# Kernel optimization log

Measured on AMD Instinct MI355X. Metric: run time of the kernel, lower is better.

## Reference

```python
import jax, jax.numpy as jnp
import numpy as np

B, T, D, H, O = 32768, 96, 7, 3, 7

def setup_inputs() -> dict:
    key = jax.random.key(0)
    ks = jax.random.split(key, 7)
    s_ih = 1.0 / np.sqrt(H)
    inp = {
        "x": jax.random.normal(ks[0], (B, T, D), dtype=jnp.float32),
        # PyTorch nn.LSTM params (gate order i,f,g,o), uniform(-1/sqrt(H), 1/sqrt(H))
        "W_ih": jax.random.uniform(ks[1], (4 * H, D), jnp.float32, -s_ih, s_ih),
        "W_hh": jax.random.uniform(ks[2], (4 * H, H), jnp.float32, -s_ih, s_ih),
        "b_ih": jax.random.uniform(ks[3], (4 * H,), jnp.float32, -s_ih, s_ih),
        "b_hh": jax.random.uniform(ks[4], (4 * H,), jnp.float32, -s_ih, s_ih),
        # nn.Linear(H*T, O*T): weight [out,in]
        "W_lin": jax.random.uniform(ks[5], (O * T, H * T), jnp.float32, -1.0 / np.sqrt(H * T), 1.0 / np.sqrt(H * T)),
        "b_lin": jax.random.uniform(ks[6], (O * T,), jnp.float32, -1.0 / np.sqrt(H * T), 1.0 / np.sqrt(H * T)),
    }
    return inp

def _lstm(x, W_ih, W_hh, b_ih, b_hh):
    b = x.shape[0]
    h0 = jnp.zeros((b, H), x.dtype)
    c0 = jnp.zeros((b, H), x.dtype)
    bias = b_ih + b_hh

    def step(carry, x_t):
        h, c = carry
        gates = x_t @ W_ih.T + h @ W_hh.T + bias  # [b, 4H]
        i, f, g, o = jnp.split(gates, 4, axis=-1)
        i = jax.nn.sigmoid(i)
        f = jax.nn.sigmoid(f)
        g = jnp.tanh(g)
        o = jax.nn.sigmoid(o)
        c = f * c + i * g
        h = o * jnp.tanh(c)
        return (h, c), h

    (_, _), hs = jax.lax.scan(step, (h0, c0), jnp.swapaxes(x, 0, 1))  # hs: [T, b, H]
    return jnp.swapaxes(hs, 0, 1)  # [b, T, H]

def reference(x, W_ih, W_hh, b_ih, b_hh, W_lin, b_lin):
    out = _lstm(x, W_ih, W_hh, b_ih, b_hh)            # [B, T, H]
    out = out.reshape(x.shape[0], -1)                  # [B, T*H]
    out = out @ W_lin.T + b_lin                        # [B, O*T]
    return out.reshape(x.shape)                        # [B, T, D]
```

## Files before the change

### kernel.cpp

```cpp
#include <hip/hip_runtime.h>
#include <stdint.h>

typedef unsigned short u16;
typedef unsigned int u32;
typedef __attribute__((ext_vector_type(8))) __bf16 bf16x8;
typedef __attribute__((ext_vector_type(4))) float f32x4;

#define B_TOT   32768
#define T_SEQ   96
#define D_IN    7
#define K_LIN   288
#define N_LIN   672
#define N_PAD   768

#define LOG2E      1.4426950408889634f
#define TWO_LOG2E  2.8853900817779268f

__device__ __forceinline__ u16 f2bf(float f) {
  u32 u = __builtin_bit_cast(u32, f);
  u += 0x7fffu + ((u >> 16) & 1u);
  return (u16)(u >> 16);
}
__device__ __forceinline__ float sig2(float zp) {
  return __builtin_amdgcn_rcpf(1.0f + __builtin_amdgcn_exp2f(-zp));
}
__device__ __forceinline__ float tanh2(float zpp) {
  return 1.0f - 2.0f * __builtin_amdgcn_rcpf(1.0f + __builtin_amdgcn_exp2f(zpp));
}
template<int Q>
__device__ __forceinline__ float qbcast(float v) {
  int i = __builtin_bit_cast(int, v);
  i = __builtin_amdgcn_update_dpp(0, i, Q * 0x55, 0xF, 0xF, true);
  return __builtin_bit_cast(float, i);
}

__global__ __launch_bounds__(256) void convert_kernel(
    const float* __restrict__ Wlin, const float* __restrict__ blin,
    u16* __restrict__ Bw, float* __restrict__ biasp)
{
  int i = blockIdx.x * 256 + threadIdx.x;
  if (i < N_PAD * K_LIN) {
    int n = i / K_LIN;
    int kk = i - n * K_LIN;
    int jm = kk / T_SEQ;
    int tm = kk - jm * T_SEQ;
    Bw[i] = f2bf((n < N_LIN) ? Wlin[n * K_LIN + tm * 3 + jm] : 0.0f);
  }
  if (i < N_PAD) biasp[i] = (i < N_LIN) ? blin[i] : 0.0f;
}

__device__ __forceinline__ void chunk4(
    const float* xc,
    float& h0, float& h1, float& h2, float& c,
    const float (&wih)[4][7], const float (&whh)[4][3], const float (&bias)[4],
    float* hv_out)
{
  float zx[4][4];
#pragma unroll
  for (int s = 0; s < 4; ++s) {
#pragma unroll
    for (int G = 0; G < 4; ++G) {
      float a = bias[G];
#pragma unroll
      for (int k = 0; k < 7; ++k) a = fmaf(xc[s * 7 + k], wih[G][k], a);
      zx[s][G] = a;
    }
  }
#pragma unroll
  for (int s = 0; s < 4; ++s) {
    float zi = fmaf(h2, whh[0][2], fmaf(h1, whh[0][1], fmaf(h0, whh[0][0], zx[s][0])));
    float zf = fmaf(h2, whh[1][2], fmaf(h1, whh[1][1], fmaf(h0, whh[1][0], zx[s][1])));
    float zg = fmaf(h2, whh[2][2], fmaf(h1, whh[2][1], fmaf(h0, whh[2][0], zx[s][2])));
    float zo = fmaf(h2, whh[3][2], fmaf(h1, whh[3][1], fmaf(h0, whh[3][0], zx[s][3])));
    float ig = sig2(zi);
    float fg = sig2(zf);
    float gg = tanh2(zg);
    float og = sig2(zo);
    c = fmaf(fg, c, ig * gg);
    float hv = og * tanh2(c * TWO_LOG2E);
    hv_out[s] = hv;
    h0 = qbcast<0>(hv);
    h1 = qbcast<1>(hv);
    h2 = qbcast<2>(hv);
  }
}

__global__ __attribute__((amdgpu_flat_work_group_size(256, 256), amdgpu_waves_per_eu(2, 2)))
void lstm_kernel(
    const float* __restrict__ x,
    const float* __restrict__ Wih, const float* __restrict__ Whh,
    const float* __restrict__ bih, const float* __restrict__ bhh,
    u16* __restrict__ hs)
{
  __shared__ float sW[132];
  const int tid = threadIdx.x;
  for (int i = tid; i < 132; i += 256) {
    float v; int row;
    if (i < 84)       { v = Wih[i];       row = i / 7; }
    else if (i < 120) { v = Whh[i - 84];  row = (i - 84) / 3; }
    else              { v = bih[i - 120] + bhh[i - 120]; row = i - 120; }
    const int G = row / 3;
    sW[i] = v * ((G == 2) ? TWO_LOG2E : LOG2E);
  }
  __syncthreads();

  const int j  = tid & 3;
  const int jj = (j < 3) ? j : 2;

  float wih[4][7], whh[4][3], bias[4];
#pragma unroll
  for (int G = 0; G < 4; ++G) {
    const int row = G * 3 + jj;
#pragma unroll
    for (int k = 0; k < 7; ++k) wih[G][k] = sW[row * 7 + k];
#pragma unroll
    for (int m = 0; m < 3; ++m) whh[G][m] = sW[84 + row * 3 + m];
    bias[G] = sW[120 + row];
  }
#pragma unroll
  for (int G = 0; G < 4; ++G) {
#pragma unroll
    for (int k = 0; k < 7; ++k) asm volatile("" : "+v"(wih[G][k]));
#pragma unroll
    for (int m = 0; m < 3; ++m) asm volatile("" : "+v"(whh[G][m]));
    asm volatile("" : "+v"(bias[G]));
  }

  const int b = (blockIdx.x * 256 + tid) >> 2;
  const float4* __restrict__ xr = (const float4*)(x + (size_t)b * (T_SEQ * D_IN));
  u16* __restrict__ hrow = hs + (size_t)b * K_LIN + jj * T_SEQ;

  float h0 = 0.f, h1 = 0.f, h2 = 0.f, c = 0.f;
  float xa[28] __attribute__((aligned(16)));
  float xb[28] __attribute__((aligned(16)));
  float hv8[8];

#pragma unroll
  for (int q = 0; q < 7; ++q) ((float4*)xa)[q] = xr[q];

#pragma unroll 1
  for (int g8 = 0; g8 < 12; ++g8) {
#pragma unroll
    for (int q = 0; q < 7; ++q) ((float4*)xb)[q] = xr[(2 * g8 + 1) * 7 + q];
    chunk4(xa, h0, h1, h2, c, wih, whh, bias, hv8);
    if (g8 < 11) {
#pragma unroll
      for (int q = 0; q < 7; ++q) ((float4*)xa)[q] = xr[(2 * g8 + 2) * 7 + q];
    }
    chunk4(xb, h0, h1, h2, c, wih, whh, bias, hv8 + 4);
    if (j < 3) {
      u32 w0, w1, w2, w3;
      asm("v_cvt_pk_bf16_f32 %0, %1, %2" : "=v"(w0) : "v"(hv8[0]), "v"(hv8[1]));
      asm("v_cvt_pk_bf16_f32 %0, %1, %2" : "=v"(w1) : "v"(hv8[2]), "v"(hv8[3]));
      asm("v_cvt_pk_bf16_f32 %0, %1, %2" : "=v"(w2) : "v"(hv8[4]), "v"(hv8[5]));
      asm("v_cvt_pk_bf16_f32 %0, %1, %2" : "=v"(w3) : "v"(hv8[6]), "v"(hv8[7]));
      uint4 pkv; pkv.x = w0; pkv.y = w1; pkv.z = w2; pkv.w = w3;
      *(uint4*)(hrow + g8 * 8) = pkv;
    }
  }
}

__device__ __forceinline__ void gload16(const u16* g, u16* l) {
  __builtin_amdgcn_global_load_lds(
      (const __attribute__((address_space(1))) void*)g,
      (__attribute__((address_space(3))) void*)l, 16, 0, 0);
}

__global__ __launch_bounds__(256) void gemm_kernel(
    const u16* __restrict__ A, const u16* __restrict__ Bw,
    const float* __restrict__ bias, float* __restrict__ C)
{
  __shared__ u16 As[128 * 32];
  __shared__ u16 Bs[128 * 32];
  const int tid  = threadIdx.x;
  const int lane = tid & 63;
  const int wid  = tid >> 6;
  const int wm = wid >> 1, wn = wid & 1;

  int bx = blockIdx.x;
  int swz = (bx & 7) * 192 + (bx >> 3);
  const int bm = swz / 6;
  const int bn = swz - bm * 6;
  const size_t m0 = (size_t)bm * 128;
  const int n0 = bn * 128;

  const int ra = tid >> 2;
  const int ca = (tid & 3) * 8;
  const u16* ga = A  + (m0 + (size_t)ra) * K_LIN + ca;
  const u16* gb = Bw + (size_t)(n0 + ra) * K_LIN + ca;
  u16* lA = &As[wid * 512];
  u16* lB = &Bs[wid * 512];

  const int l15 = lane & 15, l4 = lane >> 4;
  const u16* pAf = &As[(wm * 64 + l15) * 32 + l4 * 8];
  const u16* pBf = &Bs[(wn * 64 + l15) * 32 + l4 * 8];

  f32x4 acc[4][4] = {};

  for (int kt = 0; kt < 9; ++kt) {
    const int ko = kt * 32;
    gload16(ga + ko,               lA);
    gload16(ga + 64 * K_LIN + ko,  lA + 2048);
    gload16(gb + ko,               lB);
    gload16(gb + 64 * K_LIN + ko,  lB + 2048);
    __syncthreads();
    bf16x8 af[4], bfv[4];
#pragma unroll
    for (int i = 0; i < 4; ++i) af[i]  = *(const bf16x8*)(const void*)(pAf + i * 512);
#pragma unroll
    for (int i = 0; i < 4; ++i) bfv[i] = *(const bf16x8*)(const void*)(pBf + i * 512);
#pragma unroll
    for (int mi = 0; mi < 4; ++mi)
#pragma unroll
      for (int ni = 0; ni < 4; ++ni)
        acc[mi][ni] = __builtin_amdgcn_mfma_f32_16x16x32_bf16(af[mi], bfv[ni], acc[mi][ni], 0, 0, 0);
    __syncthreads();
  }

  float bv[4];
#pragma unroll
  for (int ni = 0; ni < 4; ++ni) bv[ni] = bias[n0 + wn * 64 + ni * 16 + l15];

#pragma unroll
  for (int mi = 0; mi < 4; ++mi) {
#pragma unroll
    for (int ni = 0; ni < 4; ++ni) {
      const int col = n0 + wn * 64 + ni * 16 + l15;
      if (col < N_LIN) {
#pragma unroll
        for (int r = 0; r < 4; ++r) {
          const size_t row = m0 + wm * 64 + mi * 16 + l4 * 4 + r;
          C[row * N_LIN + col] = acc[mi][ni][r] + bv[ni];
        }
      }
    }
  }
}

extern "C" void kernel_launch(void* const* d_in, const int* in_sizes, int n_in,
                              void* d_out, int out_size, void* d_ws, size_t ws_size,
                              hipStream_t stream) {
  const float* x    = (const float*)d_in[0];
  const float* Wih  = (const float*)d_in[1];
  const float* Whh  = (const float*)d_in[2];
  const float* bih  = (const float*)d_in[3];
  const float* bhh  = (const float*)d_in[4];
  const float* Wlin = (const float*)d_in[5];
  const float* blin = (const float*)d_in[6];
  float* out = (float*)d_out;

  u16* hs = (u16*)d_ws;
  u16* Bw = (u16*)((char*)d_ws + (size_t)B_TOT * K_LIN * 2);
  float* biasp = (float*)((char*)d_ws + (size_t)B_TOT * K_LIN * 2 + (size_t)N_PAD * K_LIN * 2);

  convert_kernel<<<(N_PAD * K_LIN + 255) / 256, 256, 0, stream>>>(Wlin, blin, Bw, biasp);
  lstm_kernel<<<(B_TOT * 4) / 256, 256, 0, stream>>>(x, Wih, Whh, bih, bhh, hs);
  gemm_kernel<<<(B_TOT / 128) * (N_PAD / 128), 256, 0, stream>>>(hs, Bw, biasp, out);
}
```

Baseline: 69.52 us.

## Stage LSTM inputs through double-buffered LDS with coalesced cooperative loads

The LSTM kernel now loads x for 64 batch rows cooperatively into a double-buffered shared-memory tile. Each load is coalesced, with 64 lanes covering consecutive rows and four waves splitting each 56-float chunk. Before, each thread read its row's x redundantly and with a strided pattern, four lanes per row. Steps are processed 8 at a time from LDS, with the next chunk's global loads issued before compute and __syncthreads per chunk. This reduces redundant global traffic but adds LDS usage, barriers, and drops the waves_per_eu hint.

```diff
diff --git a/kernel.cpp b/kernel.cpp
--- a/kernel.cpp
+++ b/kernel.cpp
@@ -49,50 +49,49 @@
   if (i < N_PAD) biasp[i] = (i < N_LIN) ? blin[i] : 0.0f;
 }
 
-__device__ __forceinline__ void chunk4(
-    const float* xc,
+__device__ __forceinline__ void steps8(
+    const float* __restrict__ xc,
     float& h0, float& h1, float& h2, float& c,
     const float (&wih)[4][7], const float (&whh)[4][3], const float (&bias)[4],
-    float* hv_out)
+    float* hv8)
 {
-  float zx[4][4];
-#pragma unroll
-  for (int s = 0; s < 4; ++s) {
-#pragma unroll
-    for (int G = 0; G < 4; ++G) {
-      float a = bias[G];
-#pragma unroll
-      for (int k = 0; k < 7; ++k) a = fmaf(xc[s * 7 + k], wih[G][k], a);
-      zx[s][G] = a;
+#pragma unroll
+  for (int s = 0; s < 8; ++s) {
+    float zi = bias[0], zf = bias[1], zg = bias[2], zo = bias[3];
+#pragma unroll
+    for (int k = 0; k < 7; ++k) {
+      const float xv = xc[s * 7 + k];
+      zi = fmaf(xv, wih[0][k], zi);
+      zf = fmaf(xv, wih[1][k], zf);
+      zg = fmaf(xv, wih[2][k], zg);
+      zo = fmaf(xv, wih[3][k], zo);
     }
-  }
-#pragma unroll
-  for (int s = 0; s < 4; ++s) {
-    float zi = fmaf(h2, whh[0][2], fmaf(h1, whh[0][1], fmaf(h0, whh[0][0], zx[s][0])));
-    float zf = fmaf(h2, whh[1][2], fmaf(h1, whh[1][1], fmaf(h0, whh[1][0], zx[s][1])));
-    float zg = fmaf(h2, whh[2][2], fmaf(h1, whh[2][1], fmaf(h0, whh[2][0], zx[s][2])));
-    float zo = fmaf(h2, whh[3][2], fmaf(h1, whh[3][1], fmaf(h0, whh[3][0], zx[s][3])));
+    zi = fmaf(h2, whh[0][2], fmaf(h1, whh[0][1], fmaf(h0, whh[0][0], zi)));
+    zf = fmaf(h2, whh[1][2], fmaf(h1, whh[1][1], fmaf(h0, whh[1][0], zf)));
+    zg = fmaf(h2, whh[2][2], fmaf(h1, whh[2][1], fmaf(h0, whh[2][0], zg)));
+    zo = fmaf(h2, whh[3][2], fmaf(h1, whh[3][1], fmaf(h0, whh[3][0], zo)));
     float ig = sig2(zi);
     float fg = sig2(zf);
     float gg = tanh2(zg);
     float og = sig2(zo);
     c = fmaf(fg, c, ig * gg);
     float hv = og * tanh2(c * TWO_LOG2E);
-    hv_out[s] = hv;
+    hv8[s] = hv;
     h0 = qbcast<0>(hv);
     h1 = qbcast<1>(hv);
     h2 = qbcast<2>(hv);
   }
 }
 
-__global__ __attribute__((amdgpu_flat_work_group_size(256, 256), amdgpu_waves_per_eu(2, 2)))
-void lstm_kernel(
+__global__ __launch_bounds__(256) void lstm_kernel(
     const float* __restrict__ x,
     const float* __restrict__ Wih, const float* __restrict__ Whh,
     const float* __restrict__ bih, const float* __restrict__ bhh,
     u16* __restrict__ hs)
 {
   __shared__ float sW[132];
+  __shared__ __align__(16) float xb[2][64 * 56];
+
   const int tid = threadIdx.x;
   for (int i = tid; i < 132; i += 256) {
     float v; int row;
@@ -126,36 +125,85 @@
     asm volatile("" : "+v"(bias[G]));
   }
 
-  const int b = (blockIdx.x * 256 + tid) >> 2;
-  const float4* __restrict__ xr = (const float4*)(x + (size_t)b * (T_SEQ * D_IN));
+  const int cs = tid & 63;
+  const int w  = tid >> 6;
+  const int b0 = blockIdx.x * 64;
+  const float* gbase = x + (size_t)(b0 + cs) * (T_SEQ * D_IN) + w * 4;
+
+  const int cc = tid >> 2;
+  const float* xc0 = &xb[0][cc * 56];
+  const float* xc1 = &xb[1][cc * 56];
+  float* xw0 = &xb[0][cs * 56 + w * 4];
+  float* xw1 = &xb[1][cs * 56 + w * 4];
+
+  const int b = b0 + cc;
   u16* __restrict__ hrow = hs + (size_t)b * K_LIN + jj * T_SEQ;
 
   float h0 = 0.f, h1 = 0.f, h2 = 0.f, c = 0.f;
-  float xa[28] __attribute__((aligned(16)));
-  float xb[28] __attribute__((aligned(16)));
   float hv8[8];
 
-#pragma unroll
-  for (int q = 0; q < 7; ++q) ((float4*)xa)[q] = xr[q];
+  {
+    const float4* gp = (const float4*)gbase;
+    float4 g0 = gp[0], g1 = gp[4], g2 = gp[8];
+    float4 g3 = {};
+    if (w < 2) g3 = gp[12];
+    float4* ld = (float4*)xw0;
+    ld[0] = g0; ld[4] = g1; ld[8] = g2;
+    if (w < 2) ld[12] = g3;
+  }
+  __syncthreads();
 
 #pragma unroll 1
-  for (int g8 = 0; g8 < 12; ++g8) {
-#pragma unroll
-    for (int q = 0; q < 7; ++q) ((float4*)xb)[q] = xr[(2 * g8 + 1) * 7 + q];
-    chunk4(xa, h0, h1, h2, c, wih, whh, bias, hv8);
-    if (g8 < 11) {
-#pragma unroll
-      for (int q = 0; q < 7; ++q) ((float4*)xa)[q] = xr[(2 * g8 + 2) * 7 + q];
+  for (int n2 = 0; n2 < 6; ++n2) {
+    const int n = n2 * 2;
+    {
+      const float4* gp = (const float4*)(gbase + (n + 1) * 56);
+      float4 g0 = gp[0], g1 = gp[4], g2 = gp[8];
+      float4 g3 = {};
+      if (w < 2) g3 = gp[12];
+      steps8(xc0, h0, h1, h2, c, wih, whh, bias, hv8);
+      __builtin_amdgcn_sched_barrier(0);
+      {
+        float4* ld = (float4*)xw1;
+        ld[0] = g0; ld[4] = g1; ld[8] = g2;
+        if (w < 2) ld[12] = g3;
+      }
+      if (j < 3) {
+        u32 w0_, w1_, w2_, w3_;
+        asm("v_cvt_pk_bf16_f32 %0, %1, %2" : "=v"(w0_) : "v"(hv8[0]), "v"(hv8[1]));
+        asm("v_cvt_pk_bf16_f32 %0, %1, %2" : "=v"(w1_) : "v"(hv8[2]), "v"(hv8[3]));
+        asm("v_cvt_pk_bf16_f32 %0, %1, %2" : "=v"(w2_) : "v"(hv8[4]), "v"(hv8[5]));
+        asm("v_cvt_pk_bf16_f32 %0, %1, %2" : "=v"(w3_) : "v"(hv8[6]), "v"(hv8[7]));
+        uint4 pkv; pkv.x = w0_; pkv.y = w1_; pkv.z = w2_; pkv.w = w3_;
+        *(uint4*)(hrow + n * 8) = pkv;
+      }
+      __syncthreads();
     }
-    chunk4(xb, h0, h1, h2, c, wih, whh, bias, hv8 + 4);
-    if (j < 3) {
-      u32 w0, w1, w2, w3;
-      asm("v_cvt_pk_bf16_f32 %0, %1, %2" : "=v"(w0) : "v"(hv8[0]), "v"(hv8[1]));
-      asm("v_cvt_pk_bf16_f32 %0, %1, %2" : "=v"(w1) : "v"(hv8[2]), "v"(hv8[3]));
-      asm("v_cvt_pk_bf16_f32 %0, %1, %2" : "=v"(w2) : "v"(hv8[4]), "v"(hv8[5]));
-      asm("v_cvt_pk_bf16_f32 %0, %1, %2" : "=v"(w3) : "v"(hv8[6]), "v"(hv8[7]));
-      uint4 pkv; pkv.x = w0; pkv.y = w1; pkv.z = w2; pkv.w = w3;
-      *(uint4*)(hrow + g8 * 8) = pkv;
+    {
+      const bool has_next = (n2 < 5);
+      float4 g0 = {}, g1 = {}, g2 = {}, g3 = {};
+      if (has_next) {
+        const float4* gp = (const float4*)(gbase + (n + 2) * 56);
+        g0 = gp[0]; g1 = gp[4]; g2 = gp[8];
+        if (w < 2) g3 = gp[12];
+      }
+      steps8(xc1, h0, h1, h2, c, wih, whh, bias, hv8);
+      __builtin_amdgcn_sched_barrier(0);
+      if (has_next) {
+        float4* ld = (float4*)xw0;
+        ld[0] = g0; ld[4] = g1; ld[8] = g2;
+        if (w < 2) ld[12] = g3;
+      }
+      if (j < 3) {
+        u32 w0_, w1_, w2_, w3_;
+        asm("v_cvt_pk_bf16_f32 %0, %1, %2" : "=v"(w0_) : "v"(hv8[0]), "v"(hv8[1]));
+        asm("v_cvt_pk_bf16_f32 %0, %1, %2" : "=v"(w1_) : "v"(hv8[2]), "v"(hv8[3]));
+        asm("v_cvt_pk_bf16_f32 %0, %1, %2" : "=v"(w2_) : "v"(hv8[4]), "v"(hv8[5]));
+        asm("v_cvt_pk_bf16_f32 %0, %1, %2" : "=v"(w3_) : "v"(hv8[6]), "v"(hv8[7]));
+        uint4 pkv; pkv.x = w0_; pkv.y = w1_; pkv.z = w2_; pkv.w = w3_;
+        *(uint4*)(hrow + (n + 1) * 8) = pkv;
+      }
+      __syncthreads();
     }
   }
 }
@@ -254,6 +302,6 @@
   float* biasp = (float*)((char*)d_ws + (size_t)B_TOT * K_LIN * 2 + (size_t)N_PAD * K_LIN * 2);
 
   convert_kernel<<<(N_PAD * K_LIN + 255) / 256, 256, 0, stream>>>(Wlin, blin, Bw, biasp);
-  lstm_kernel<<<(B_TOT * 4) / 256, 256, 0, stream>>>(x, Wih, Whh, bih, bhh, hs);
+  lstm_kernel<<<B_TOT / 64, 256, 0, stream>>>(x, Wih, Whh, bih, bhh, hs);
   gemm_kernel<<<(B_TOT / 128) * (N_PAD / 128), 256, 0, stream>>>(hs, Bw, biasp, out);
 }
```

New measurement: 70.33 us. Within noise of the previous version (+1.2%).
